# Kernel optimization log

Measured on AMD Instinct MI355X. Metric: run time of the kernel, lower is better.

## Reference

```python
import jax, jax.numpy as jnp
import numpy as np
import math

N_HEAD = 16
D_MODEL = 1024
ATT_DIM = D_MODEL // N_HEAD


def setup_inputs() -> dict:
    key = jax.random.key(0)
    ks = jax.random.split(key, 11)
    B, T, D = 2, 2048, D_MODEL
    s = 1.0 / math.sqrt(D)
    return {
        "q": jax.random.normal(ks[0], (B, T, D), jnp.float32),
        "k": jax.random.normal(ks[1], (B, T, D), jnp.float32),
        "v": jax.random.normal(ks[2], (B, T, D), jnp.float32),
        "Wq": jax.random.normal(ks[3], (D, D), jnp.float32) * s,
        "bq": jnp.zeros((D,), jnp.float32),
        "Wk": jax.random.normal(ks[4], (D, D), jnp.float32) * s,
        "bk": jnp.zeros((D,), jnp.float32),
        "Wv": jax.random.normal(ks[5], (D, D), jnp.float32) * s,
        "bv": jnp.zeros((D,), jnp.float32),
        "Wo": jax.random.normal(ks[6], (D, D), jnp.float32) * s,
        "bo": jnp.zeros((D,), jnp.float32),
    }


def reference(q, k, v, Wq, bq, Wk, bk, Wv, bv, Wo, bo):
    B, T, D = q.shape
    H, hd = N_HEAD, ATT_DIM
    # Linear projections (torch Linear: x @ W.T + b)
    qh = (q @ Wq.T + bq).reshape(B, T, H, hd).transpose(0, 2, 1, 3)  # [B,H,T,hd]
    kh = (k @ Wk.T + bk).reshape(B, T, H, hd).transpose(0, 2, 1, 3)
    vh = (v @ Wv.T + bv).reshape(B, T, H, hd).transpose(0, 2, 1, 3)
    scale = 1.0 / math.sqrt(hd)
    score = jnp.einsum("bhqd,bhkd->bhqk", qh, kh) * scale  # [B,H,T,T]
    attn = jax.nn.softmax(score, axis=-1)
    out = jnp.einsum("bhqk,bhkd->bhqd", attn, vh)  # [B,H,T,hd]
    out = out.transpose(0, 2, 1, 3).reshape(B, T, D)
    return out @ Wo.T + bo
```

## Files before the change

kernel.cpp:

```cpp
#include <hip/hip_runtime.h>


typedef __attribute__((ext_vector_type(8))) short bf16x8;
typedef __attribute__((ext_vector_type(4))) float f32x4;

#define E22 ((size_t)1 << 22)
#define E20 ((size_t)1 << 20)

__device__ __forceinline__ unsigned short f2bf(float x) {
    unsigned int u = __float_as_uint(x);
    u += 0x7fffu + ((u >> 16) & 1u);
    return (unsigned short)(u >> 16);
}
__device__ __forceinline__ unsigned int pk2bf(float a, float b) {
    return __builtin_amdgcn_perm(__float_as_uint(a), __float_as_uint(b), 0x03020706u);
}
__device__ __forceinline__ void gl16(const void* g, void* l) {
    __builtin_amdgcn_global_load_lds(
        (const __attribute__((address_space(1))) void*)g,
        (__attribute__((address_space(3))) void*)l, 16, 0, 0);
}
__device__ __forceinline__ f32x4 mfma16(bf16x8 a, bf16x8 b, f32x4 c) {
    return __builtin_amdgcn_mfma_f32_16x16x32_bf16(a, b, c, 0, 0, 0);
}

__global__ __launch_bounds__(256)
void split_all(const float* __restrict__ q, const float* __restrict__ k,
               const float* __restrict__ v, const float* __restrict__ wq,
               const float* __restrict__ wk, const float* __restrict__ wv,
               const float* __restrict__ wo, unsigned short* __restrict__ ws)
{
    const size_t t = (size_t)blockIdx.x * 256 + threadIdx.x;
    const size_t e = t * 4;
    const float* src; unsigned short* dst; size_t off;
    if (e < 3 * E22) {
        const unsigned int which = (unsigned int)(e >> 22);
        src = which == 0 ? q : (which == 1 ? k : v);
        off = e & (E22 - 1);
        dst = ws + (size_t)which * E22;
    } else {
        const size_t e2 = e - 3 * E22;
        const unsigned int which = (unsigned int)(e2 >> 20);
        off = e2 & (E20 - 1);
        src = which == 0 ? wq : (which == 1 ? wk : (which == 2 ? wv : wo));
        dst = ws + 3 * E22 + (size_t)which * E20;
    }
    const float4 xv = *(const float4*)(src + off);
    ushort4 h4;
    h4.x = f2bf(xv.x); h4.y = f2bf(xv.y); h4.z = f2bf(xv.z); h4.w = f2bf(xv.w);
    *(ushort4*)(dst + off) = h4;
}

__global__ __launch_bounds__(256)
void gemm_qkv(const unsigned short* __restrict__ Xall,
              const unsigned short* __restrict__ Wcat,
              const float* __restrict__ bq, const float* __restrict__ bk,
              const float* __restrict__ bv, unsigned short* __restrict__ Qhp,
              unsigned short* __restrict__ Khp, unsigned short* __restrict__ Vtp)
{
    __shared__ unsigned short Xs[3 * 4096], Ws[3 * 4096];
    const int tid = threadIdx.x;
    const int w = tid >> 6, ln = tid & 63;
    const int quad = ln >> 4, L = ln & 15;
    const int wy = w >> 1, wx = w & 1;

    const int bid = blockIdx.x;
    const int xcd = bid & 7, j = bid >> 3;
    const int gg = xcd * 12 + (j >> 3);
    const int which = gg >> 5, m_i = gg & 31, n_i = j & 7;
    const int m0 = m_i * 128;

    const unsigned short* X = Xall + (size_t)which * E22;
    const unsigned short* W = Wcat + ((size_t)which * 1024 + n_i * 128) * 1024;
    const float* bp = which == 0 ? bq : (which == 1 ? bk : bv);
    unsigned short* outp = which == 0 ? Qhp : (which == 1 ? Khp : Vtp);
    const float qscale = which == 0 ? 0.18033688011f : 1.0f;

    const int ci0 = ln, ci1 = 64 + ln;
    const int row0 = w * 32 + (ci0 >> 2), row1 = w * 32 + (ci1 >> 2);
    const int gc0 = (ci0 & 3) ^ ((row0 >> 1) & 3);
    const int gc1 = (ci1 & 3) ^ ((row1 >> 1) & 3);
    const int lb0 = w * 2048, lb1 = w * 2048 + 1024;
    const unsigned short* Xbp = X + (size_t)m0 * 1024;
    const size_t gx0 = (size_t)row0 * 1024 + gc0 * 8;
    const size_t gx1 = (size_t)row1 * 1024 + gc1 * 8;

    f32x4 acc[4][4];
#pragma unroll
    for (int i = 0; i < 4; ++i)
#pragma unroll
        for (int jj = 0; jj < 4; ++jj) { f32x4 z = {0.f,0.f,0.f,0.f}; acc[i][jj] = z; }

#define QSTAGE(k0_, bo_)                                                       \
    do {                                                                       \
        gl16(Xbp + gx0 + (k0_), (char*)Xs + (bo_) + lb0);                      \
        gl16(W   + gx0 + (k0_), (char*)Ws + (bo_) + lb0);                      \
        gl16(Xbp + gx1 + (k0_), (char*)Xs + (bo_) + lb1);                      \
        gl16(W   + gx1 + (k0_), (char*)Ws + (bo_) + lb1);                      \
    } while (0)

#define QCOMP(eo_)                                                             \
    do {                                                                       \
        const unsigned short* Xc = Xs + (eo_);                                 \
        const unsigned short* Wc = Ws + (eo_);                                 \
        bf16x8 ah[4], bh[4];                                                   \
        _Pragma("unroll")                                                      \
        for (int mt = 0; mt < 4; ++mt) {                                       \
            const int row = wy * 64 + mt * 16 + L;                             \
            ah[mt] = *(const bf16x8*)(Xc + row * 32 +                          \
                                      ((quad ^ ((row >> 1) & 3)) * 8));        \
        }                                                                      \
        _Pragma("unroll")                                                      \
        for (int nt = 0; nt < 4; ++nt) {                                       \
            const int row = wx * 64 + nt * 16 + L;                             \
            bh[nt] = *(const bf16x8*)(Wc + row * 32 +                          \
                                      ((quad ^ ((row >> 1) & 3)) * 8));        \
        }                                                                      \
        _Pragma("unroll")                                                      \
        for (int mt = 0; mt < 4; ++mt)                                         \
            _Pragma("unroll")                                                  \
            for (int nt = 0; nt < 4; ++nt)                                     \
                acc[mt][nt] = mfma16(ah[mt], bh[nt], acc[mt][nt]);             \
    } while (0)

    QSTAGE(0, 0);
    QSTAGE(32, 8192);

    int cur = 0;
    for (int kt = 0; kt < 31; ++kt) {
        asm volatile("s_waitcnt vmcnt(4)" ::: "memory");
        __builtin_amdgcn_s_barrier();
        asm volatile("" ::: "memory");
        if (kt < 30) {
            int st = cur + 2; if (st >= 3) st -= 3;
            QSTAGE((kt + 2) * 32, st * 8192);
        }
        QCOMP(cur * 4096);
        cur = (cur == 2) ? 0 : cur + 1;
    }
    asm volatile("s_waitcnt vmcnt(0)" ::: "memory");
    __builtin_amdgcn_s_barrier();
    asm volatile("" ::: "memory");
    QCOMP(cur * 4096);
#undef QSTAGE
#undef QCOMP

#pragma unroll
    for (int mt = 0; mt < 4; ++mt)
#pragma unroll
        for (int nt = 0; nt < 4; ++nt) {
            const int gm0 = m0 + wy * 64 + mt * 16 + quad * 4;
            const int bn  = n_i * 128 + wx * 64 + nt * 16 + L;
            const float bvv = bp[bn];
            const int hh = bn >> 6, dd = bn & 63;
            if (which < 2) {
#pragma unroll
                for (int r = 0; r < 4; ++r) {
                    const int gm = gm0 + r;
                    const int bb = gm >> 11, tt = gm & 2047;
                    outp[((size_t)(bb * 16 + hh) * 2048 + tt) * 64 + dd] =
                        f2bf((acc[mt][nt][r] + bvv) * qscale);
                }
            } else {
                const int bb = gm0 >> 11, t0 = gm0 & 2047;
                ushort4 pk;
                pk.x = f2bf(acc[mt][nt][0] + bvv);
                pk.y = f2bf(acc[mt][nt][1] + bvv);
                pk.z = f2bf(acc[mt][nt][2] + bvv);
                pk.w = f2bf(acc[mt][nt][3] + bvv);
                *(ushort4*)(outp + ((size_t)(bb * 16 + hh) * 64 + dd) * 2048 + t0) = pk;
            }
        }
}

__global__ __launch_bounds__(256)
void gemm_out(const unsigned short* __restrict__ X, const unsigned short* __restrict__ W,
              const float* __restrict__ bias, float* __restrict__ outp)
{
    __shared__ unsigned short Xs[3 * 4096], Ws[3 * 2048];
    const int tid = threadIdx.x;
    const int w = tid >> 6, ln = tid & 63;
    const int quad = ln >> 4, L = ln & 15;

    const int bid = blockIdx.x;
    const int xcd = bid & 7, j = bid >> 3;
    const int m0 = (xcd * 4 + (j >> 4)) * 128;
    const int n0 = (j & 15) * 64;

    const int cix0 = ln, cix1 = 64 + ln;
    const int rowx0 = w * 32 + (cix0 >> 2), rowx1 = w * 32 + (cix1 >> 2);
    const int gcx0 = (cix0 & 3) ^ ((rowx0 >> 1) & 3);
    const int gcx1 = (cix1 & 3) ^ ((rowx1 >> 1) & 3);
    const int roww = w * 16 + (ln >> 2);
    const int gcw = (ln & 3) ^ ((roww >> 1) & 3);
    const size_t gxx0 = (size_t)(m0 + rowx0) * 1024 + gcx0 * 8;
    const size_t gxx1 = (size_t)(m0 + rowx1) * 1024 + gcx1 * 8;
    const size_t gww  = (size_t)(n0 + roww) * 1024 + gcw * 8;

    f32x4 acc[2][4];
#pragma unroll
    for (int i = 0; i < 2; ++i)
#pragma unroll
        for (int jj = 0; jj < 4; ++jj) { f32x4 z = {0.f,0.f,0.f,0.f}; acc[i][jj] = z; }

#define OSTAGE(k0_, bf_)                                                       \
    do {                                                                       \
        gl16(X + gxx0 + (k0_), (char*)Xs + (bf_) * 8192 + w * 2048);           \
        gl16(X + gxx1 + (k0_), (char*)Xs + (bf_) * 8192 + w * 2048 + 1024);    \
        gl16(W + gww  + (k0_), (char*)Ws + (bf_) * 4096 + w * 1024);           \
    } while (0)

#define OCOMP(bf_)                                                             \
    do {                                                                       \
        const unsigned short* Xc = Xs + (bf_) * 4096;                          \
        const unsigned short* Wc = Ws + (bf_) * 2048;                          \
        bf16x8 ah[2], bh[4];                                                   \
        _Pragma("unroll")                                                      \
        for (int mt = 0; mt < 2; ++mt) {                                       \
            const int row = w * 32 + mt * 16 + L;                              \
            ah[mt] = *(const bf16x8*)(Xc + row * 32 +                          \
                                      ((quad ^ ((row >> 1) & 3)) * 8));        \
        }                                                                      \
        _Pragma("unroll")                                                      \
        for (int nt = 0; nt < 4; ++nt) {                                       \
            const int row = nt * 16 + L;                                       \
            bh[nt] = *(const bf16x8*)(Wc + row * 32 +                          \
                                      ((quad ^ ((row >> 1) & 3)) * 8));        \
        }                                                                      \
        _Pragma("unroll")                                                      \
        for (int mt = 0; mt < 2; ++mt)                                         \
            _Pragma("unroll")                                                  \
            for (int nt = 0; nt < 4; ++nt)                                     \
                acc[mt][nt] = mfma16(ah[mt], bh[nt], acc[mt][nt]);             \
    } while (0)

    OSTAGE(0, 0);
    OSTAGE(32, 1);

    int cur = 0;
    for (int kt = 0; kt < 31; ++kt) {
        asm volatile("s_waitcnt vmcnt(3)" ::: "memory");
        __builtin_amdgcn_s_barrier();
        asm volatile("" ::: "memory");
        if (kt < 30) {
            int st = cur + 2; if (st >= 3) st -= 3;
            OSTAGE((kt + 2) * 32, st);
        }
        OCOMP(cur);
        cur = (cur == 2) ? 0 : cur + 1;
    }
    asm volatile("s_waitcnt vmcnt(0)" ::: "memory");
    __builtin_amdgcn_s_barrier();
    asm volatile("" ::: "memory");
    OCOMP(cur);
#undef OSTAGE
#undef OCOMP

#pragma unroll
    for (int mt = 0; mt < 2; ++mt)
#pragma unroll
        for (int nt = 0; nt < 4; ++nt) {
            const int gm0 = m0 + w * 32 + mt * 16 + quad * 4;
            const int gn  = n0 + nt * 16 + L;
            const float bvv = bias[gn];
#pragma unroll
            for (int r = 0; r < 4; ++r)
                outp[(size_t)(gm0 + r) * 1024 + gn] = acc[mt][nt][r] + bvv;
        }
}

__global__ __launch_bounds__(256, 2)
void flash(const unsigned short* __restrict__ Qh, const unsigned short* __restrict__ Kh,
           const unsigned short* __restrict__ Vt, unsigned short* __restrict__ A)
{
    __shared__ unsigned short KVs[16384];
    __shared__ unsigned short PT[4 * 64 * 72];
    const int tid = threadIdx.x;
    const int w = tid >> 6, ln = tid & 63;
    const int quad = ln >> 4, L = ln & 15;
    const int wq = w & 1, wk = w >> 1;

    const int bid = blockIdx.x;
    const int xcd = bid & 7, j = bid >> 3;
    const int bh_i = xcd * 4 + (j & 3);
    const int qt = j >> 2;
    const int b = bh_i >> 4, h = bh_i & 15;

    const unsigned short* Qb = Qh + ((size_t)bh_i * 2048 + qt * 128 + wq * 64) * 64;
    const unsigned short* Kb = Kh + (size_t)bh_i * 2048 * 64;
    const unsigned short* Vb = Vt + (size_t)bh_i * 64 * 2048;

    bf16x8 bq[4][2];
#pragma unroll
    for (int nt = 0; nt < 4; ++nt)
#pragma unroll
        for (int kc = 0; kc < 2; ++kc)
            bq[nt][kc] = *(const bf16x8*)(Qb + (nt * 16 + L) * 64 + kc * 32 + quad * 8);

    const short one_bf = (short)0x3F80;
    bf16x8 bone = {one_bf, one_bf, one_bf, one_bf, one_bf, one_bf, one_bf, one_bf};

    f32x4 o[4][4];
    f32x4 lacc[4];
#pragma unroll
    for (int mtd = 0; mtd < 4; ++mtd)
#pragma unroll
        for (int nt = 0; nt < 4; ++nt) { f32x4 z = {0.f,0.f,0.f,0.f}; o[mtd][nt] = z; }
#pragma unroll
    for (int nt = 0; nt < 4; ++nt) { f32x4 z = {0.f,0.f,0.f,0.f}; lacc[nt] = z; }

    unsigned short* Pw = PT + w * 64 * 72;

    const int ci0 = (w * 2 + 0) * 64 + ln, ci1 = (w * 2 + 1) * 64 + ln;
    const int rr0 = ci0 >> 3, rr1 = ci1 >> 3;
    const int gc0 = (ci0 & 7) ^ (rr0 & 7), gc1 = (ci1 & 7) ^ (rr1 & 7);

#define STAGE(kt_, buf_)                                                        \
    do {                                                                        \
        gl16(Kb + (size_t)((kt_) * 64 + rr0) * 64 + gc0 * 8,                    \
             (char*)KVs + (buf_) * 8192 + (w * 2 + 0) * 1024);                  \
        gl16(Kb + (size_t)((kt_) * 64 + rr1) * 64 + gc1 * 8,                    \
             (char*)KVs + (buf_) * 8192 + (w * 2 + 1) * 1024);                  \
        gl16(Vb + (size_t)rr0 * 2048 + (kt_) * 64 + gc0 * 8,                    \
             (char*)KVs + 16384 + (buf_) * 8192 + (w * 2 + 0) * 1024);          \
        gl16(Vb + (size_t)rr1 * 2048 + (kt_) * 64 + gc1 * 8,                    \
             (char*)KVs + 16384 + (buf_) * 8192 + (w * 2 + 1) * 1024);          \
    } while (0)

    STAGE(0, 0);

    for (int kt = 0; kt < 32; ++kt) {
        const int cur = kt & 1;
        __syncthreads();
        if (kt < 31) STAGE(kt + 1, cur ^ 1);

        const unsigned short* Ksb = KVs + cur * 4096;
        const unsigned short* Vsb = KVs + 8192 + cur * 4096;

        bf16x8 ak[2][2];
#pragma unroll
        for (int mt = 0; mt < 2; ++mt)
#pragma unroll
            for (int kc = 0; kc < 2; ++kc) {
                const int row = wk * 32 + mt * 16 + L;
                ak[mt][kc] = *(const bf16x8*)(Ksb + row * 64 + (((kc * 4 + quad) ^ (L & 7)) * 8));
            }

        f32x4 s[2][4];
#pragma unroll
        for (int mt = 0; mt < 2; ++mt)
#pragma unroll
            for (int nt = 0; nt < 4; ++nt) {
                f32x4 z = {0.f,0.f,0.f,0.f};
                z = mfma16(ak[mt][0], bq[nt][0], z);
                z = mfma16(ak[mt][1], bq[nt][1], z);
                s[mt][nt] = z;
            }

#pragma unroll
        for (int mt = 0; mt < 2; ++mt)
#pragma unroll
            for (int nt = 0; nt < 4; ++nt) {
                const float p0 = __builtin_amdgcn_exp2f(s[mt][nt][0]);
                const float p1 = __builtin_amdgcn_exp2f(s[mt][nt][1]);
                const float p2 = __builtin_amdgcn_exp2f(s[mt][nt][2]);
                const float p3 = __builtin_amdgcn_exp2f(s[mt][nt][3]);
                uint2 pk2;
                pk2.x = pk2bf(p0, p1);
                pk2.y = pk2bf(p2, p3);
                *(uint2*)(Pw + (nt * 16 + L) * 72 + mt * 16 + quad * 4) = pk2;
            }
        asm volatile("s_waitcnt lgkmcnt(0)" ::: "memory");

        bf16x8 av[4], pb[4];
#pragma unroll
        for (int mtd = 0; mtd < 4; ++mtd) {
            const int row = mtd * 16 + L;
            av[mtd] = *(const bf16x8*)(Vsb + row * 64 + (((wk * 4 + quad) ^ (L & 7)) * 8));
        }
#pragma unroll
        for (int nt = 0; nt < 4; ++nt)
            pb[nt] = *(const bf16x8*)(Pw + (nt * 16 + L) * 72 + quad * 8);

#pragma unroll
        for (int mtd = 0; mtd < 4; ++mtd)
#pragma unroll
            for (int nt = 0; nt < 4; ++nt)
                o[mtd][nt] = mfma16(av[mtd], pb[nt], o[mtd][nt]);
#pragma unroll
        for (int nt = 0; nt < 4; ++nt)
            lacc[nt] = mfma16(bone, pb[nt], lacc[nt]);
    }
#undef STAGE

    __syncthreads();
    float* Rb = (float*)KVs;
    float* Lb = (float*)PT;
    if (wk == 1) {
#pragma unroll
        for (int mtd = 0; mtd < 4; ++mtd)
#pragma unroll
            for (int nt = 0; nt < 4; ++nt)
                *(f32x4*)(Rb + wq * 4096 + (mtd * 4 + nt) * 256 + ln * 4) = o[mtd][nt];
#pragma unroll
        for (int nt = 0; nt < 4; ++nt)
            *(f32x4*)(Lb + wq * 1024 + nt * 256 + ln * 4) = lacc[nt];
    }
    __syncthreads();
    if (wk == 0) {
#pragma unroll
        for (int mtd = 0; mtd < 4; ++mtd)
#pragma unroll
            for (int nt = 0; nt < 4; ++nt)
                o[mtd][nt] += *(const f32x4*)(Rb + wq * 4096 + (mtd * 4 + nt) * 256 + ln * 4);
#pragma unroll
        for (int nt = 0; nt < 4; ++nt)
            lacc[nt] += *(const f32x4*)(Lb + wq * 1024 + nt * 256 + ln * 4);

#pragma unroll
        for (int nt = 0; nt < 4; ++nt) {
            const float inv = 1.0f / lacc[nt][0];
            const int qrow = b * 2048 + qt * 128 + wq * 64 + nt * 16 + L;
#pragma unroll
            for (int mtd = 0; mtd < 4; ++mtd) {
                const int d0 = mtd * 16 + quad * 4;
                ushort4 pk;
                pk.x = f2bf(o[mtd][nt][0] * inv);
                pk.y = f2bf(o[mtd][nt][1] * inv);
                pk.z = f2bf(o[mtd][nt][2] * inv);
                pk.w = f2bf(o[mtd][nt][3] * inv);
                *(ushort4*)(A + (size_t)qrow * 1024 + h * 64 + d0) = pk;
            }
        }
    }
}

extern "C" void kernel_launch(void* const* d_in, const int* in_sizes, int n_in,
                              void* d_out, int out_size, void* d_ws, size_t ws_size,
                              hipStream_t stream) {
    const float* q  = (const float*)d_in[0];
    const float* k  = (const float*)d_in[1];
    const float* v  = (const float*)d_in[2];
    const float* Wq = (const float*)d_in[3];
    const float* bq = (const float*)d_in[4];
    const float* Wk = (const float*)d_in[5];
    const float* bk = (const float*)d_in[6];
    const float* Wv = (const float*)d_in[7];
    const float* bv = (const float*)d_in[8];
    const float* Wo = (const float*)d_in[9];
    const float* bo = (const float*)d_in[10];

    unsigned short* W = (unsigned short*)d_ws;
    unsigned short *Xall = W;
    unsigned short *Wcat = W + 3 * E22;
    unsigned short *Wob  = Wcat + 3 * E20;
    unsigned short *Qhp  = W + 4 * E22;
    unsigned short *Khp  = W + 5 * E22;
    unsigned short *Vtp  = W + 6 * E22;
    unsigned short *A    = W;

    split_all<<<16384, 256, 0, stream>>>(q, k, v, Wq, Wk, Wv, Wo, W);

    gemm_qkv<<<768, 256, 0, stream>>>(Xall, Wcat, bq, bk, bv, Qhp, Khp, Vtp);

    flash<<<512, 256, 0, stream>>>(Qhp, Khp, Vtp, A);

    gemm_out<<<512, 256, 0, stream>>>(A, Wob, bo, (float*)d_out);
}
```

Measured before the change: 215.6 us.

## Keep softmax probabilities in registers and permute V loads to match layout

The exponentiated scores are packed straight from the S accumulator registers into the B operand of the PV MFMA, so the per-iteration LDS round trip (write P, waitcnt, read back) and its shared buffer go away. To make this work, the reduction index is permuted consistently: V tiles are now read as two 8-byte halves at XOR-swizzled offsets that match the register order of P. This cuts LDS traffic and shared memory use, which may also raise occupancy. The cost is that V reads become two narrower LDS loads instead of one 16-byte load, and the row-sum reduction changes to a scalar-per-lane scheme.

```diff
diff --git a/kernel.cpp b/kernel.cpp
--- a/kernel.cpp
+++ b/kernel.cpp
@@ -3,6 +3,8 @@
 
 typedef __attribute__((ext_vector_type(8))) short bf16x8;
 typedef __attribute__((ext_vector_type(4))) float f32x4;
+typedef __attribute__((ext_vector_type(4))) unsigned int u32x4;
+typedef __attribute__((ext_vector_type(2))) unsigned long long u64x2;
 
 #define E22 ((size_t)1 << 22)
 #define E20 ((size_t)1 << 20)
@@ -274,7 +276,7 @@
            const unsigned short* __restrict__ Vt, unsigned short* __restrict__ A)
 {
     __shared__ unsigned short KVs[16384];
-    __shared__ unsigned short PT[4 * 64 * 72];
+    __shared__ float Lsc[2 * 4 * 64];
     const int tid = threadIdx.x;
     const int w = tid >> 6, ln = tid & 63;
     const int quad = ln >> 4, L = ln & 15;
@@ -309,11 +311,13 @@
 #pragma unroll
     for (int nt = 0; nt < 4; ++nt) { f32x4 z = {0.f,0.f,0.f,0.f}; lacc[nt] = z; }
 
-    unsigned short* Pw = PT + w * 64 * 72;
-
     const int ci0 = (w * 2 + 0) * 64 + ln, ci1 = (w * 2 + 1) * 64 + ln;
     const int rr0 = ci0 >> 3, rr1 = ci1 >> 3;
     const int gc0 = (ci0 & 7) ^ (rr0 & 7), gc1 = (ci1 & 7) ^ (rr1 & 7);
+
+    const int rbv = L & 7;
+    const int vg0 = ((wk * 4 + (quad >> 1)) ^ rbv) * 8 + (quad & 1) * 4;
+    const int vg1 = ((wk * 4 + 2 + (quad >> 1)) ^ rbv) * 8 + (quad & 1) * 4;
 
 #define STAGE(kt_, buf_)                                                        \
     do {                                                                        \
@@ -357,45 +361,44 @@
                 s[mt][nt] = z;
             }
 
-#pragma unroll
-        for (int mt = 0; mt < 2; ++mt)
-#pragma unroll
-            for (int nt = 0; nt < 4; ++nt) {
-                const float p0 = __builtin_amdgcn_exp2f(s[mt][nt][0]);
-                const float p1 = __builtin_amdgcn_exp2f(s[mt][nt][1]);
-                const float p2 = __builtin_amdgcn_exp2f(s[mt][nt][2]);
-                const float p3 = __builtin_amdgcn_exp2f(s[mt][nt][3]);
-                uint2 pk2;
-                pk2.x = pk2bf(p0, p1);
-                pk2.y = pk2bf(p2, p3);
-                *(uint2*)(Pw + (nt * 16 + L) * 72 + mt * 16 + quad * 4) = pk2;
-            }
-        asm volatile("s_waitcnt lgkmcnt(0)" ::: "memory");
-
-        bf16x8 av[4], pb[4];
+        bf16x8 pbx[4];
+#pragma unroll
+        for (int nt = 0; nt < 4; ++nt) {
+            u32x4 pd;
+            pd.x = pk2bf(__builtin_amdgcn_exp2f(s[0][nt][0]),
+                         __builtin_amdgcn_exp2f(s[0][nt][1]));
+            pd.y = pk2bf(__builtin_amdgcn_exp2f(s[0][nt][2]),
+                         __builtin_amdgcn_exp2f(s[0][nt][3]));
+            pd.z = pk2bf(__builtin_amdgcn_exp2f(s[1][nt][0]),
+                         __builtin_amdgcn_exp2f(s[1][nt][1]));
+            pd.w = pk2bf(__builtin_amdgcn_exp2f(s[1][nt][2]),
+                         __builtin_amdgcn_exp2f(s[1][nt][3]));
+            pbx[nt] = __builtin_bit_cast(bf16x8, pd);
+        }
+
+        bf16x8 av[4];
 #pragma unroll
         for (int mtd = 0; mtd < 4; ++mtd) {
-            const int row = mtd * 16 + L;
-            av[mtd] = *(const bf16x8*)(Vsb + row * 64 + (((wk * 4 + quad) ^ (L & 7)) * 8));
-        }
+            const unsigned short* Vr = Vsb + (mtd * 16 + L) * 64;
+            u64x2 t;
+            t.x = *(const unsigned long long*)(Vr + vg0);
+            t.y = *(const unsigned long long*)(Vr + vg1);
+            av[mtd] = __builtin_bit_cast(bf16x8, t);
+        }
+
+#pragma unroll
+        for (int mtd = 0; mtd < 4; ++mtd)
+#pragma unroll
+            for (int nt = 0; nt < 4; ++nt)
+                o[mtd][nt] = mfma16(av[mtd], pbx[nt], o[mtd][nt]);
 #pragma unroll
         for (int nt = 0; nt < 4; ++nt)
-            pb[nt] = *(const bf16x8*)(Pw + (nt * 16 + L) * 72 + quad * 8);
-
-#pragma unroll
-        for (int mtd = 0; mtd < 4; ++mtd)
-#pragma unroll
-            for (int nt = 0; nt < 4; ++nt)
-                o[mtd][nt] = mfma16(av[mtd], pb[nt], o[mtd][nt]);
-#pragma unroll
-        for (int nt = 0; nt < 4; ++nt)
-            lacc[nt] = mfma16(bone, pb[nt], lacc[nt]);
+            lacc[nt] = mfma16(bone, pbx[nt], lacc[nt]);
     }
 #undef STAGE
 
     __syncthreads();
     float* Rb = (float*)KVs;
-    float* Lb = (float*)PT;
     if (wk == 1) {
 #pragma unroll
         for (int mtd = 0; mtd < 4; ++mtd)
@@ -404,7 +407,7 @@
                 *(f32x4*)(Rb + wq * 4096 + (mtd * 4 + nt) * 256 + ln * 4) = o[mtd][nt];
 #pragma unroll
         for (int nt = 0; nt < 4; ++nt)
-            *(f32x4*)(Lb + wq * 1024 + nt * 256 + ln * 4) = lacc[nt];
+            Lsc[wq * 256 + nt * 64 + ln] = lacc[nt][0];
     }
     __syncthreads();
     if (wk == 0) {
@@ -413,13 +416,11 @@
 #pragma unroll
             for (int nt = 0; nt < 4; ++nt)
                 o[mtd][nt] += *(const f32x4*)(Rb + wq * 4096 + (mtd * 4 + nt) * 256 + ln * 4);
-#pragma unroll
-        for (int nt = 0; nt < 4; ++nt)
-            lacc[nt] += *(const f32x4*)(Lb + wq * 1024 + nt * 256 + ln * 4);
 
 #pragma unroll
         for (int nt = 0; nt < 4; ++nt) {
-            const float inv = 1.0f / lacc[nt][0];
+            const float lsum = lacc[nt][0] + Lsc[wq * 256 + nt * 64 + ln];
+            const float inv = 1.0f / lsum;
             const int qrow = b * 2048 + qt * 128 + wq * 64 + nt * 16 + L;
 #pragma unroll
             for (int mtd = 0; mtd < 4; ++mtd) {
```

New measurement: 212.4 us. About the same (-1.5%).
